# Optimization experiments

Measured on AMD Instinct MI355X. Metric: run time of the kernel, lower is better.

## Reference

```python
import jax, jax.numpy as jnp
import numpy as np

B, T, M, D, DOUT = 2, 10000, 100000, 128, 128


def setup_inputs() -> dict:
    key = jax.random.key(0)
    k1, k2, k3, k4, k5, k6 = jax.random.split(key, 6)
    x_1st = jax.random.normal(k1, (B, T, 2, D), dtype=jnp.float32)
    x_2nd = jax.random.normal(k2, (B, M, 4, D), dtype=jnp.float32)  # unused in forward math
    edge = jax.random.randint(k3, (2, M), 0, T, dtype=jnp.int32)
    A_masked = jax.random.normal(k4, (B, 1, M), dtype=jnp.float32)
    W = jax.random.normal(k5, (DOUT, D), dtype=jnp.float32) / jnp.sqrt(jnp.float32(D))
    b = jax.random.normal(k6, (DOUT,), dtype=jnp.float32) * 0.01
    return {"x_1st": x_1st, "x_2nd": x_2nd, "edge": edge, "A_masked": A_masked, "W": W, "b": b}


def reference(x_1st, x_2nd, edge, A_masked, W, b):
    node_in, node_out = edge[0], edge[1]  # (M,)
    w = A_masked[:, 0, :, None]  # (B, M, 1) edge weights

    def node_message_passing(x):  # x: (B, T, d)
        msg = x[:, node_out, :] * w                        # gather + edge-weight mul: (B, M, d)
        upd = jnp.zeros_like(x).at[:, node_in, :].add(msg)  # scatter_add into T nodes
        return x + upd

    x_neg = node_message_passing(x_1st[:, :, 0, :])
    x_pos = node_message_passing(x_1st[:, :, 1, :])
    x = jnp.stack([x_neg, x_pos], axis=2)  # (B, T, 2, d)
    return jnp.einsum("btcd,od->btco", x, W) + b  # node_layer Linear
```

## Files before the change

kernel.cpp:

```cpp
#include <hip/hip_runtime.h>
#include <hip/hip_bf16.h>

#define BB    2
#define TT    10000
#define MM    100000
#define DD    128
#define DOUTN 128
#define NROWS (BB * TT * 2)
#define NTILES (NROWS / 16)
#define WPITCH 136

typedef float  f32x4  __attribute__((ext_vector_type(4)));
typedef short  bf16x8 __attribute__((ext_vector_type(8)));

static __device__ __forceinline__ short f2bf(float f) {
    union { float f; unsigned u; } v; v.f = f;
    unsigned r = v.u + 0x7fffu + ((v.u >> 16) & 1u);
    return (short)(r >> 16);
}

__global__ __launch_bounds__(256)
void gemm_y_kernel(const float* __restrict__ X, const float* __restrict__ W,
                   float* __restrict__ y) {
    __shared__ __align__(16) short Wb[DOUTN * WPITCH];

    const int tid = threadIdx.x;
    {
        const int n  = tid >> 1;
        const int kh = (tid & 1) * 64;
        const float* wp = W + n * DD + kh;
        short* dst = &Wb[n * WPITCH + kh];
#pragma unroll
        for (int e = 0; e < 8; ++e) {
            float4 a = *(const float4*)(wp + e * 8);
            float4 b = *(const float4*)(wp + e * 8 + 4);
            bf16x8 t;
            t[0] = f2bf(a.x); t[1] = f2bf(a.y); t[2] = f2bf(a.z); t[3] = f2bf(a.w);
            t[4] = f2bf(b.x); t[5] = f2bf(b.y); t[6] = f2bf(b.z); t[7] = f2bf(b.w);
            *(bf16x8*)(dst + e * 8) = t;
        }
    }
    __syncthreads();

    const int lane = tid & 63;
    const int wid  = tid >> 6;
    const int l15  = lane & 15;
    const int q    = lane >> 4;
    const int tile = blockIdx.x * 4 + wid;

    bf16x8 bfrag[8][4];
#pragma unroll
    for (int ot = 0; ot < 8; ++ot)
#pragma unroll
        for (int s = 0; s < 4; ++s)
            bfrag[ot][s] = *(const bf16x8*)&Wb[(ot * 16 + l15) * WPITCH + s * 32 + q * 8];

    const float* xp = X + (size_t)(tile * 16 + l15) * DD + q * 8;
    bf16x8 afrag[4];
#pragma unroll
    for (int s = 0; s < 4; ++s) {
        float4 a0 = *(const float4*)(xp + s * 32);
        float4 a1 = *(const float4*)(xp + s * 32 + 4);
        bf16x8 t;
        t[0] = f2bf(a0.x); t[1] = f2bf(a0.y); t[2] = f2bf(a0.z); t[3] = f2bf(a0.w);
        t[4] = f2bf(a1.x); t[5] = f2bf(a1.y); t[6] = f2bf(a1.z); t[7] = f2bf(a1.w);
        afrag[s] = t;
    }

    f32x4 acc[8];
#pragma unroll
    for (int ot = 0; ot < 8; ++ot) acc[ot] = (f32x4){0.f, 0.f, 0.f, 0.f};
#pragma unroll
    for (int s = 0; s < 4; ++s)
#pragma unroll
        for (int ot = 0; ot < 8; ++ot)
            acc[ot] = __builtin_amdgcn_mfma_f32_16x16x32_bf16(afrag[s], bfrag[ot][s], acc[ot], 0, 0, 0);

#pragma unroll
    for (int ot = 0; ot < 8; ++ot) {
        const int col = ot * 16 + l15;
#pragma unroll
        for (int r = 0; r < 4; ++r) {
            const int row = tile * 16 + q * 4 + r;
            y[(size_t)row * DOUTN + col] = acc[ot][r];
        }
    }
}

__global__ __launch_bounds__(256)
void hist_kernel(const int* __restrict__ edge, int* __restrict__ cnt) {
    const int m = blockIdx.x * 256 + threadIdx.x;
    if (m < MM) atomicAdd(&cnt[edge[m]], 1);
}

#define SCAN_T 1024
#define SCAN_CH 10
__global__ __launch_bounds__(SCAN_T)
void scan_kernel(int* __restrict__ cur) {
    __shared__ int sh[SCAN_T];
    const int tid = threadIdx.x;
    int vals[SCAN_CH];
    int sum = 0;
    const int base_i = tid * SCAN_CH;
#pragma unroll
    for (int j = 0; j < SCAN_CH; ++j) {
        const int i = base_i + j;
        const int v = (i < TT) ? cur[i] : 0;
        vals[j] = v; sum += v;
    }
    sh[tid] = sum;
    __syncthreads();
    for (int off = 1; off < SCAN_T; off <<= 1) {
        const int v = (tid >= off) ? sh[tid - off] : 0;
        __syncthreads();
        sh[tid] += v;
        __syncthreads();
    }
    int run = (tid == 0) ? 0 : sh[tid - 1];
#pragma unroll
    for (int j = 0; j < SCAN_CH; ++j) {
        const int i = base_i + j;
        if (i < TT) { cur[i] = run; run += vals[j]; }
    }
}

__global__ __launch_bounds__(256)
void fill_kernel(const int* __restrict__ edge, int* __restrict__ cur,
                 int* __restrict__ bucket) {
    const int m = blockIdx.x * 256 + threadIdx.x;
    if (m < MM) {
        const int p = atomicAdd(&cur[edge[m]], 1);
        bucket[p] = m;
    }
}

__global__ __launch_bounds__(256)
void gather_kernel(const float* __restrict__ y, const int* __restrict__ edge,
                   const float* __restrict__ Am, const int* __restrict__ cur_end,
                   const int* __restrict__ bucket, const float* __restrict__ bias,
                   float* __restrict__ out) {
    const int wid  = threadIdx.x >> 6;
    const int lane = threadIdx.x & 63;
    const int r = blockIdx.x * 4 + wid;
    if (r >= NROWS) return;
    const int c = r & 1;
    const int t = (r >> 1) % TT;
    const int b = r / (2 * TT);

    float2 acc = ((const float2*)(y + (size_t)r * DD))[lane];
    const float2 bs = ((const float2*)bias)[lane];

    const int*   esrc = edge + MM;
    const float* Amb  = Am + b * MM;
    const float* yb   = y + (size_t)b * TT * 2 * DD + (size_t)c * DD;

    const int end   = cur_end[t];
    const int start = (t == 0) ? 0 : cur_end[t - 1];
    for (int e = start; e < end; ++e) {
        const int m    = bucket[e];
        const int nout = esrc[m];
        const float w  = Amb[m];
        const float2 v = ((const float2*)(yb + (size_t)nout * 2 * DD))[lane];
        acc.x += w * v.x;
        acc.y += w * v.y;
    }
    float2 o; o.x = acc.x + bs.x; o.y = acc.y + bs.y;
    ((float2*)(out + (size_t)r * DD))[lane] = o;
}

extern "C" void kernel_launch(void* const* d_in, const int* in_sizes, int n_in,
                              void* d_out, int out_size, void* d_ws, size_t ws_size,
                              hipStream_t stream) {
    const float* x1   = (const float*)d_in[0];
    const int*   edge = (const int*)d_in[2];
    const float* Am   = (const float*)d_in[3];
    const float* W    = (const float*)d_in[4];
    const float* bias = (const float*)d_in[5];
    float* out = (float*)d_out;

    float* y      = (float*)d_ws;
    int*   cur    = (int*)d_ws + (size_t)NROWS * DOUTN;
    int*   bucket = cur + TT;

    hipMemsetAsync(cur, 0, TT * sizeof(int), stream);
    hist_kernel<<<(MM + 255) / 256, 256, 0, stream>>>(edge, cur);
    scan_kernel<<<1, SCAN_T, 0, stream>>>(cur);
    fill_kernel<<<(MM + 255) / 256, 256, 0, stream>>>(edge, cur, bucket);

    gemm_y_kernel<<<NTILES / 4, 256, 0, stream>>>(x1, W, y);

    gather_kernel<<<(NROWS + 3) / 4, 256, 0, stream>>>(y, edge, Am, cur, bucket, bias, out);
}
```

Before: 549.3 us.

## Gather all four rows per target node and batch edge metadata via readlane

```diff
diff --git a/kernel.cpp b/kernel.cpp
--- a/kernel.cpp
+++ b/kernel.cpp
@@ -139,33 +139,55 @@
                    const float* __restrict__ Am, const int* __restrict__ cur_end,
                    const int* __restrict__ bucket, const float* __restrict__ bias,
                    float* __restrict__ out) {
-    const int wid  = threadIdx.x >> 6;
     const int lane = threadIdx.x & 63;
-    const int r = blockIdx.x * 4 + wid;
-    if (r >= NROWS) return;
-    const int c = r & 1;
-    const int t = (r >> 1) % TT;
-    const int b = r / (2 * TT);
-
-    float2 acc = ((const float2*)(y + (size_t)r * DD))[lane];
-    const float2 bs = ((const float2*)bias)[lane];
-
-    const int*   esrc = edge + MM;
-    const float* Amb  = Am + b * MM;
-    const float* yb   = y + (size_t)b * TT * 2 * DD + (size_t)c * DD;
+    const int t    = blockIdx.x * 4 + (threadIdx.x >> 6);
 
     const int end   = cur_end[t];
     const int start = (t == 0) ? 0 : cur_end[t - 1];
-    for (int e = start; e < end; ++e) {
-        const int m    = bucket[e];
-        const int nout = esrc[m];
-        const float w  = Amb[m];
-        const float2 v = ((const float2*)(yb + (size_t)nout * 2 * DD))[lane];
-        acc.x += w * v.x;
-        acc.y += w * v.y;
-    }
-    float2 o; o.x = acc.x + bs.x; o.y = acc.y + bs.y;
-    ((float2*)(out + (size_t)r * DD))[lane] = o;
+
+    const float* yb0 = y + (size_t)t * 256;
+    const float* yb1 = y + (size_t)(TT + t) * 256;
+    float2 a00 = ((const float2*)yb0)[lane];
+    float2 a01 = ((const float2*)(yb0 + 128))[lane];
+    float2 a10 = ((const float2*)yb1)[lane];
+    float2 a11 = ((const float2*)(yb1 + 128))[lane];
+
+    const int* esrc = edge + MM;
+
+    for (int base = start; base < end; base += 64) {
+        const int n = min(end - base, 64);
+        int nout = 0; float w0 = 0.f, w1 = 0.f;
+        if (lane < n) {
+            const int m = bucket[base + lane];
+            nout = esrc[m];
+            w0   = Am[m];
+            w1   = Am[MM + m];
+        }
+        for (int e = 0; e < n; ++e) {
+            const int   no  = __builtin_amdgcn_readlane(nout, e);
+            const float ww0 = __uint_as_float(__builtin_amdgcn_readlane(__float_as_uint(w0), e));
+            const float ww1 = __uint_as_float(__builtin_amdgcn_readlane(__float_as_uint(w1), e));
+            const float* p0 = y + (size_t)no * 256;
+            const float* p1 = y + (size_t)(TT + no) * 256;
+            const float2 v00 = ((const float2*)p0)[lane];
+            const float2 v01 = ((const float2*)(p0 + 128))[lane];
+            const float2 v10 = ((const float2*)p1)[lane];
+            const float2 v11 = ((const float2*)(p1 + 128))[lane];
+            a00.x += ww0 * v00.x; a00.y += ww0 * v00.y;
+            a01.x += ww0 * v01.x; a01.y += ww0 * v01.y;
+            a10.x += ww1 * v10.x; a10.y += ww1 * v10.y;
+            a11.x += ww1 * v11.x; a11.y += ww1 * v11.y;
+        }
+    }
+
+    const float2 bs = ((const float2*)bias)[lane];
+    float* o0 = out + (size_t)t * 256;
+    float* o1 = out + (size_t)(TT + t) * 256;
+    float2 r;
+    r.x = a00.x + bs.x; r.y = a00.y + bs.y; ((float2*)o0)[lane]         = r;
+    r.x = a01.x + bs.x; r.y = a01.y + bs.y; ((float2*)(o0 + 128))[lane] = r;
+    r.x = a10.x + bs.x; r.y = a10.y + bs.y; ((float2*)o1)[lane]         = r;
+    r.x = a11.x + bs.x; r.y = a11.y + bs.y; ((float2*)(o1 + 128))[lane] = r;
 }
 
 extern "C" void kernel_launch(void* const* d_in, const int* in_sizes, int n_in,
@@ -189,5 +211,5 @@
 
     gemm_y_kernel<<<NTILES / 4, 256, 0, stream>>>(x1, W, y);
 
-    gather_kernel<<<(NROWS + 3) / 4, 256, 0, stream>>>(y, edge, Am, cur, bucket, bias, out);
-}
+    gather_kernel<<<TT / 4, 256, 0, stream>>>(y, edge, Am, cur, bucket, bias, out);
+}
```

New measurement: 524.1 us. 4.6% less time.
